# Optimization experiments

Hardware: AMD Instinct MI355X
Metric: run time of the kernel (lower is better)

## Reference

```python
import jax, jax.numpy as jnp
import numpy as np

B, NG, K_NN = 8, 4096, 3          # graphs, nodes per graph, knn k
CHEB_K = 4                        # SGWT/Chebyshev order K
IN_CH, HID, M, OUT_CH = 32, 64, 100, 16
N = B * NG
E_PPI = 600
BIG = 1e9


def knn_edges(x, n_graphs, n_per, k):
    """Per-graph knn_graph (no self loops). Returns global (src, dst), edges grouped per target node."""
    xg = x.reshape(n_graphs, n_per, -1)
    sq = jnp.sum(xg * xg, axis=-1)                                   # [B, n]
    d = sq[:, :, None] + sq[:, None, :] - 2.0 * jnp.einsum('bic,bjc->bij', xg, xg)
    d = d + BIG * jnp.eye(n_per, dtype=x.dtype)                      # exclude self
    idx = jax.lax.top_k(-d, k)[1]                                    # [B, n, k] neighbor ids
    offs = (jnp.arange(n_graphs) * n_per)[:, None, None]
    src = (idx + offs).reshape(-1)
    dst = jnp.broadcast_to(jnp.arange(n_per)[None, :, None] + offs, (n_graphs, n_per, k)).reshape(-1)
    return src, dst


def cheb_conv(x, src, dst, w, W, b, n):
    """SGWT/Chebyshev conv: sum_k T_k(L~) x W_k with L~ = -D^-1/2 A D^-1/2 (lambda_max=2)."""
    deg = jax.ops.segment_sum(w, dst, num_segments=n)
    dn = jnp.where(deg > 0, jax.lax.rsqrt(jnp.maximum(deg, 1e-12)), 0.0)
    wn = w * dn[dst] * dn[src]

    def lap(v):
        return -jax.ops.segment_sum(wn[:, None] * v[src], dst, num_segments=n)

    Z_prev = x
    out = x @ W[0]
    Z_cur = lap(x)
    out = out + Z_cur @ W[1]
    for kk in range(2, W.shape[0]):
        Z_next = 2.0 * lap(Z_cur) - Z_prev
        out = out + Z_next @ W[kk]
        Z_prev, Z_cur = Z_cur, Z_next
    return out + b


def graph_norm(x, alpha, gamma, beta, n_graphs, n_per, eps=1e-5):
    xg = x.reshape(n_graphs, n_per, -1)
    mean = xg.mean(axis=1, keepdims=True)
    sub = xg - alpha * mean
    var = (sub * sub).mean(axis=1, keepdims=True)
    out = gamma * sub * jax.lax.rsqrt(var + eps) + beta
    return out.reshape(x.shape)


def edge_conv(x, src, dst, W, b, n):
    """EdgeConv: max_j MLP([x_i, x_j - x_i])."""
    feat = jnp.concatenate([x[dst], x[src] - x[dst]], axis=1)
    h = jax.nn.relu(feat @ W + b)
    agg = jax.ops.segment_max(h, dst, num_segments=n)
    return jnp.where(jnp.isfinite(agg), agg, 0.0)


def mlp3(x, w1, b1, w2, b2, w3, b3):
    h = jax.nn.selu(x @ w1 + b1)
    h = jax.nn.selu(h @ w2 + b2)
    return h @ w3 + b3


def setup_inputs():
    key = jax.random.key(0)
    ks = jax.random.split(key, 32)

    def p(i, shape):
        fan_in = shape[-2] if len(shape) >= 2 else shape[-1]
        return jax.random.normal(ks[i], shape, jnp.float32) / np.sqrt(fan_in)

    inp = {
        'x': jax.random.normal(ks[0], (N, IN_CH), jnp.float32),
        'edge_weight': jax.random.uniform(ks[1], (N * K_NN,), jnp.float32),
        'batch': jnp.repeat(jnp.arange(B), NG),
        'connect': jax.random.randint(ks[2], (2, E_PPI), 0, M),
        # conv0 (SGWT) params
        'W0': p(3, (CHEB_K, IN_CH, HID)), 'b0': jnp.zeros((HID,), jnp.float32),
        # GraphNorm
        'gn_alpha': jnp.ones((HID,), jnp.float32), 'gn_gamma': jnp.ones((HID,), jnp.float32), 'gn_beta': jnp.zeros((HID,), jnp.float32),
        # conv1 (SGWT) params -> m*4
        'W1': p(4, (CHEB_K, HID, 4 * M)), 'b1c': jnp.zeros((4 * M,), jnp.float32),
        # fc1: 4m -> 2m -> m -> m
        'f1w1': p(5, (4 * M, 2 * M)), 'f1b1': jnp.zeros((2 * M,), jnp.float32),
        'f1w2': p(6, (2 * M, M)), 'f1b2': jnp.zeros((M,), jnp.float32),
        'f1w3': p(7, (M, M)), 'f1b3': jnp.zeros((M,), jnp.float32),
        # conv2 (PPIEdgeConv): 2*in_ch -> hidden
        'W2': p(8, (2 * IN_CH, HID)), 'b2': jnp.zeros((HID,), jnp.float32),
        # conv3 (DynamicEdgeConv): 2*hidden -> hidden
        'W3': p(9, (2 * HID, HID)), 'b3': jnp.zeros((HID,), jnp.float32),
        # fc2: h -> h/2 -> h/4 -> out
        'f2w1': p(10, (HID, HID // 2)), 'f2b1': jnp.zeros((HID // 2,), jnp.float32),
        'f2w2': p(11, (HID // 2, HID // 4)), 'f2b2': jnp.zeros((HID // 4,), jnp.float32),
        'f2w3': p(12, (HID // 4, OUT_CH)), 'f2b3': jnp.zeros((OUT_CH,), jnp.float32),
    }
    return inp


def reference(x, edge_weight, batch, connect, W0, b0, gn_alpha, gn_gamma, gn_beta,
              W1, b1c, f1w1, f1b1, f1w2, f1b2, f1w3, f1b3,
              W2, b2, W3, b3, f2w1, f2b1, f2w2, f2b2, f2w3, f2b3):
    n = x.shape[0]
    # knn on raw features -> SGWT conv0 -> GraphNorm
    src, dst = knn_edges(x, B, NG, K_NN)
    u = cheb_conv(x, src, dst, edge_weight, W0, b0, n)
    u = graph_norm(u, gn_alpha, gn_gamma, gn_beta, B, NG)
    # knn on hidden features -> SGWT conv1 -> fc1
    src, dst = knn_edges(u, B, NG, K_NN)
    u = cheb_conv(u, src, dst, edge_weight, W1, b1c, n)
    u = mlp3(u, f1w1, f1b1, f1w2, f1b2, f1w3, f1b3)                   # [N, M]
    # DiffPool-style soft assignment pooling
    S = jax.nn.softmax(u, axis=-1).reshape(B, NG, M)
    Xd = x.reshape(B, NG, IN_CH)
    pooled = jnp.einsum('bnm,bnc->bmc', S, Xd) / S.sum(axis=1)[:, :, None]
    xp = pooled.reshape(B * M, IN_CH)
    # PPIEdgeConv over fixed 'connect' graph replicated per pooled graph
    offs = (jnp.arange(B) * M)[:, None]
    psrc = (connect[0][None, :] + offs).reshape(-1)
    pdst = (connect[1][None, :] + offs).reshape(-1)
    h = edge_conv(xp, psrc, pdst, W2, b2, B * M)                      # [B*M, HID]
    # DynamicEdgeConv: knn(k=3) on features
    ksrc, kdst = knn_edges(h, B, M, K_NN)
    y = edge_conv(h, ksrc, kdst, W3, b3, B * M)
    z = h + y
    v = mlp3(z, f2w1, f2b1, f2w2, f2b2, f2w3, f2b3)                   # [B*M, OUT_CH]
    return u, v
```

## Files before the change

### kernel.cpp

```cpp
#include <hip/hip_runtime.h>
#include <hip/hip_bf16.h>
#include <math.h>

#define DEVFN static __device__ __forceinline__

DEVFN int clampi(int v, int lo, int hi){ return v < lo ? lo : (v > hi ? hi : v); }


__global__ void k_zero(float* __restrict__ p, int n){
  int i = blockIdx.x*256 + threadIdx.x;
  if (i < n) p[i] = 0.f;
}

__global__ void k_filli(int* __restrict__ p, int n, int v){
  int i = blockIdx.x*256 + threadIdx.x;
  if (i < n) p[i] = v;
}

__global__ void k_fillf(float* __restrict__ p, int n, float v){
  int i = blockIdx.x*256 + threadIdx.x;
  if (i < n) p[i] = v;
}

__global__ void k_sqnorm(const float* __restrict__ x, float* __restrict__ sq, int n, int C){
  int i = blockIdx.x*256 + threadIdx.x;
  if (i >= n) return;
  const float* r = x + (size_t)i*C;
  float s = 0.f;
  for (int c = 0; c < C; ++c){ float v = r[c]; s += v*v; }
  sq[i] = s;
}


DEVFN void top3i(float d, int j, float& d0, float& d1, float& d2, int& i0, int& i1, int& i2){
  if (d < d2){
    if (d < d1){
      d2 = d1; i2 = i1;
      if (d < d0){ d1 = d0; i1 = i0; d0 = d; i0 = j; }
      else       { d1 = d;  i1 = j; }
    } else { d2 = d; i2 = j; }
  }
}

DEVFN void top3t(float d, int j, float& d0, float& d1, float& d2, int& j0, int& j1, int& j2){
  if (d < d2 || (d == d2 && j < j2)){
    if (d < d1 || (d == d1 && j < j1)){
      d2 = d1; j2 = j1;
      if (d < d0 || (d == d0 && j < j0)){ d1 = d0; j1 = j0; d0 = d; j0 = j; }
      else { d1 = d; j1 = j; }
    } else { d2 = d; j2 = j; }
  }
}


template<int C, int TJ>
__global__ __launch_bounds__(64) void k_knn(
    const float* __restrict__ x, const float* __restrict__ sq,
    int n_per, int bpg, int nsplit, int csize,
    float* __restrict__ partd, int* __restrict__ parti)
{
  int bid  = blockIdx.x;
  int s    = bid % nsplit;
  int b2i  = bid / nsplit;
  int g    = b2i / bpg;
  int tile = b2i % bpg;
  int tid  = threadIdx.x;
  int i0 = tile*128 + tid;
  int i1 = i0 + 64;
  const float* xg = x  + (size_t)g*n_per*C;
  const float* sg = sq + (size_t)g*n_per;
  bool a0 = i0 < n_per, a1 = i1 < n_per;
  float xi0[C], xi1[C];
  float q0 = 0.f, q1 = 0.f;
  if (a0){
    #pragma unroll
    for (int c = 0; c < C; ++c) xi0[c] = xg[(size_t)i0*C + c];
    q0 = sg[i0];
  } else {
    #pragma unroll
    for (int c = 0; c < C; ++c) xi0[c] = 0.f;
  }
  if (a1){
    #pragma unroll
    for (int c = 0; c < C; ++c) xi1[c] = xg[(size_t)i1*C + c];
    q1 = sg[i1];
  } else {
    #pragma unroll
    for (int c = 0; c < C; ++c) xi1[c] = 0.f;
  }
  __shared__ float xs[TJ*C];
  __shared__ float ss[TJ];
  float d00 = __builtin_inff(), d01 = __builtin_inff(), d02 = __builtin_inff();
  float d10 = __builtin_inff(), d11 = __builtin_inff(), d12 = __builtin_inff();
  int n00 = 0, n01 = 0, n02 = 0;
  int n10 = 0, n11 = 0, n12 = 0;

  int jbase = s*csize;
  int jend  = min(n_per, jbase + csize);
  for (int t0 = jbase; t0 < jend; t0 += TJ){
    int lim = min(TJ, jend - t0);
    __syncthreads();
    for (int idx = tid; idx < lim*C; idx += 64) xs[idx] = xg[(size_t)t0*C + idx];
    for (int idx = tid; idx < lim;   idx += 64) ss[idx] = sg[t0 + idx];
    __syncthreads();
    for (int jj = 0; jj < lim; ++jj){
      const float4* xr = (const float4*)(xs + jj*C);
      float p0a=0,p0b=0,p0c=0,p0d=0;
      float p1a=0,p1b=0,p1c=0,p1d=0;
      #pragma unroll
      for (int c4 = 0; c4 < C/4; ++c4){
        float4 w = xr[c4];
        p0a += xi0[4*c4+0]*w.x; p0b += xi0[4*c4+1]*w.y;
        p0c += xi0[4*c4+2]*w.z; p0d += xi0[4*c4+3]*w.w;
        p1a += xi1[4*c4+0]*w.x; p1b += xi1[4*c4+1]*w.y;
        p1c += xi1[4*c4+2]*w.z; p1d += xi1[4*c4+3]*w.w;
      }
      int j = t0 + jj;
      float dv0 = q0 + ss[jj] - 2.f*((p0a+p0b)+(p0c+p0d));
      float dv1 = q1 + ss[jj] - 2.f*((p1a+p1b)+(p1c+p1d));
      if (a0 && j != i0) top3i(dv0, j, d00,d01,d02, n00,n01,n02);
      if (a1 && j != i1) top3i(dv1, j, d10,d11,d12, n10,n11,n12);
    }
  }
  if (a0){
    size_t o = ((size_t)(g*n_per + i0)*nsplit + s)*3;
    partd[o+0]=d00; partd[o+1]=d01; partd[o+2]=d02;
    parti[o+0]=n00; parti[o+1]=n01; parti[o+2]=n02;
  }
  if (a1){
    size_t o = ((size_t)(g*n_per + i1)*nsplit + s)*3;
    partd[o+0]=d10; partd[o+1]=d11; partd[o+2]=d12;
    parti[o+0]=n10; parti[o+1]=n11; parti[o+2]=n12;
  }
}


template<int C, int TJ>
__global__ __launch_bounds__(64) void k_knn1r(
    const float* __restrict__ x, const float* __restrict__ sq,
    int n_per, int bpg, int nsplit, int csize,
    float* __restrict__ partd, int* __restrict__ parti)
{
  int bid  = blockIdx.x;
  int s    = bid % nsplit;
  int b2i  = bid / nsplit;
  int g    = b2i / bpg;
  int tile = b2i % bpg;
  int tid  = threadIdx.x;
  int i0 = tile*64 + tid;
  const float* xg = x  + (size_t)g*n_per*C;
  const float* sg = sq + (size_t)g*n_per;
  float xi0[C];
  #pragma unroll
  for (int c = 0; c < C; ++c) xi0[c] = xg[(size_t)i0*C + c];
  float q0 = sg[i0];

  __shared__ float xs[TJ*C];
  __shared__ float ss[TJ];
  float d00 = __builtin_inff(), d01 = __builtin_inff(), d02 = __builtin_inff();
  int n00 = 0, n01 = 0, n02 = 0;

  int jbase = s*csize;
  int jend  = min(n_per, jbase + csize);
  for (int t0 = jbase; t0 < jend; t0 += TJ){
    int lim = min(TJ, jend - t0);
    __syncthreads();
    for (int idx = tid; idx < lim*C; idx += 64) xs[idx] = xg[(size_t)t0*C + idx];
    for (int idx = tid; idx < lim;   idx += 64) ss[idx] = sg[t0 + idx];
    __syncthreads();
    for (int jj = 0; jj < lim; ++jj){
      const float4* xr = (const float4*)(xs + jj*C);
      float p0a=0,p0b=0,p0c=0,p0d=0;
      #pragma unroll
      for (int c4 = 0; c4 < C/4; ++c4){
        float4 w = xr[c4];
        p0a += xi0[4*c4+0]*w.x; p0b += xi0[4*c4+1]*w.y;
        p0c += xi0[4*c4+2]*w.z; p0d += xi0[4*c4+3]*w.w;
      }
      int j = t0 + jj;
      float dv0 = q0 + ss[jj] - 2.f*((p0a+p0b)+(p0c+p0d));
      if (j != i0) top3i(dv0, j, d00,d01,d02, n00,n01,n02);
    }
  }
  size_t o = ((size_t)(g*n_per + i0)*nsplit + s)*3;
  partd[o+0]=d00; partd[o+1]=d01; partd[o+2]=d02;
  parti[o+0]=n00; parti[o+1]=n01; parti[o+2]=n02;
}

__global__ void k_knnmerge(const float* __restrict__ partd, const int* __restrict__ parti,
                           int n_total, int n_per, int nsplit, int* __restrict__ nbr)
{
  int row = blockIdx.x*256 + threadIdx.x;
  if (row >= n_total) return;
  float d0 = __builtin_inff(), d1 = __builtin_inff(), d2 = __builtin_inff();
  int j0 = 0, j1 = 0, j2 = 0;
  for (int s = 0; s < nsplit; ++s){
    for (int q = 0; q < 3; ++q){
      size_t o = ((size_t)row*nsplit + s)*3 + q;
      float d = partd[o]; int j = parti[o];
      top3t(d, j, d0,d1,d2, j0,j1,j2);
    }
  }
  int g = row / n_per;
  nbr[row*3+0] = g*n_per + clampi(j0, 0, n_per-1);
  nbr[row*3+1] = g*n_per + clampi(j1, 0, n_per-1);
  nbr[row*3+2] = g*n_per + clampi(j2, 0, n_per-1);
}


__global__ void k_chebwn(const float* __restrict__ w, const int* __restrict__ nbr,
                         float* __restrict__ wn, int ne, int n){
  int e = blockIdx.x*256 + threadIdx.x;
  if (e >= ne) return;
  int i = e/3;
  int s = clampi(nbr[e], 0, n-1);
  float sd = w[3*i] + w[3*i+1] + w[3*i+2];
  float sv = w[3*s] + w[3*s+1] + w[3*s+2];
  float dnd = (sd > 0.f) ? 1.f / sqrtf(fmaxf(sd, 1e-12f)) : 0.f;
  float dns = (sv > 0.f) ? 1.f / sqrtf(fmaxf(sv, 1e-12f)) : 0.f;
  wn[e] = w[e] * dnd * dns;
}

template<int C>
__global__ void k_lap(const float* __restrict__ v, const float* __restrict__ zp,
                      const float* __restrict__ wn, const int* __restrict__ nbr,
                      float* __restrict__ out, int total, float aa, float bb)
{
  int idx = blockIdx.x*256 + threadIdx.x;
  if (idx >= total) return;
  int i = idx / C;
  int c = idx - i*C;
  int e = i*3;
  int nmax = total / C;
  int s0 = clampi(nbr[e+0], 0, nmax-1);
  int s1 = clampi(nbr[e+1], 0, nmax-1);
  int s2 = clampi(nbr[e+2], 0, nmax-1);
  float s = wn[e+0]*v[(size_t)s0*C + c]
          + wn[e+1]*v[(size_t)s1*C + c]
          + wn[e+2]*v[(size_t)s2*C + c];
  float r = -aa*s;
  if (bb != 0.f) r += bb*zp[idx];
  out[idx] = r;
}


struct In4 { const float* p0; const float* p1; const float* p2; const float* p3; };

template<int ACT, int NIN>
__global__ __launch_bounds__(256) void k_mm(
    In4 ins, const float* __restrict__ W,
    const float* __restrict__ bias, float* __restrict__ out,
    int nrows, int cin, int cout)
{
  __shared__ float inl[64][65];
  __shared__ float wl[64][64];
  int r0 = blockIdx.x * 64;
  int c0 = blockIdx.y * 64;
  int tid = threadIdx.x;
  int tr = tid & 15, tc = tid >> 4;
  float acc[4][4] = {{0,0,0,0},{0,0,0,0},{0,0,0,0},{0,0,0,0}};
  const float* inp[4] = {ins.p0, ins.p1, ins.p2, ins.p3};
  for (int ni = 0; ni < NIN; ++ni){
    const float* A = inp[ni];
    const float* Wb = W + (size_t)ni*cin*cout;
    for (int k0 = 0; k0 < cin; k0 += 64){
      int klim = min(64, cin - k0);
      __syncthreads();
      for (int idx = tid; idx < 64*64; idx += 256){
        int rr = idx >> 6, kk = idx & 63;
        float v = 0.f;
        if (r0 + rr < nrows && kk < klim) v = A[(size_t)(r0+rr)*cin + k0 + kk];
        inl[rr][kk] = v;
      }
      for (int idx = tid; idx < 64*64; idx += 256){
        int kk = idx >> 6, jj = idx & 63;
        float v = 0.f;
        if (kk < klim && c0 + jj < cout) v = Wb[(size_t)(k0+kk)*cout + c0 + jj];
        wl[kk][jj] = v;
      }
      __syncthreads();
      for (int kk = 0; kk < 64; ++kk){
        float4 wv = *(const float4*)&wl[kk][tc*4];
        float a0v = inl[tr*4+0][kk];
        float a1v = inl[tr*4+1][kk];
        float a2v = inl[tr*4+2][kk];
        float a3v = inl[tr*4+3][kk];
        acc[0][0] += a0v*wv.x; acc[0][1] += a0v*wv.y; acc[0][2] += a0v*wv.z; acc[0][3] += a0v*wv.w;
        acc[1][0] += a1v*wv.x; acc[1][1] += a1v*wv.y; acc[1][2] += a1v*wv.z; acc[1][3] += a1v*wv.w;
        acc[2][0] += a2v*wv.x; acc[2][1] += a2v*wv.y; acc[2][2] += a2v*wv.z; acc[2][3] += a2v*wv.w;
        acc[3][0] += a3v*wv.x; acc[3][1] += a3v*wv.y; acc[3][2] += a3v*wv.z; acc[3][3] += a3v*wv.w;
      }
    }
  }
  #pragma unroll
  for (int q = 0; q < 4; ++q){
    int r = r0 + tr*4 + q;
    if (r >= nrows) continue;
    #pragma unroll
    for (int p = 0; p < 4; ++p){
      int j = c0 + tc*4 + p;
      if (j >= cout) continue;
      float v = acc[q][p] + bias[j];
      if (ACT == 1) v = fmaxf(v, 0.f);
      if (ACT == 2) v = 1.0507009873554805f * (v > 0.f ? v : 1.6732632423543772f * expm1f(v));
      out[(size_t)r*cout + j] = v;
    }
  }
}


__global__ void k_gnstat(const float* __restrict__ x, float* __restrict__ msum_p,
                         float* __restrict__ m2sum_p)
{
  int g = blockIdx.x >> 4, chunk = blockIdx.x & 15;
  int c = threadIdx.x & 63, q = threadIdx.x >> 6;
  const float* xg = x + (size_t)g*4096*64;
  int nb = chunk*256;
  float s1 = 0.f, s2 = 0.f;
  for (int n = nb + q; n < nb + 256; n += 4){
    float v = xg[(size_t)n*64 + c];
    s1 += v; s2 += v*v;
  }
  __shared__ float r1[4][64], r2[4][64];
  r1[q][c] = s1; r2[q][c] = s2;
  __syncthreads();
  if (q == 0){
    msum_p [(g*16 + chunk)*64 + c] = r1[0][c]+r1[1][c]+r1[2][c]+r1[3][c];
    m2sum_p[(g*16 + chunk)*64 + c] = r2[0][c]+r2[1][c]+r2[2][c]+r2[3][c];
  }
}

__global__ void k_gnapply(float* __restrict__ x, const float* __restrict__ msum_p,
                          const float* __restrict__ m2sum_p,
                          const float* __restrict__ alpha, const float* __restrict__ gamma,
                          const float* __restrict__ beta)
{
  int idx = blockIdx.x*256 + threadIdx.x;
  if (idx >= 32768*64) return;
  int c = idx & 63;
  int node = idx >> 6;
  int g = node >> 12;
  float ms = 0.f, m2 = 0.f;
  for (int ch = 0; ch < 16; ++ch){
    ms += msum_p [(g*16 + ch)*64 + c];
    m2 += m2sum_p[(g*16 + ch)*64 + c];
  }
  float m  = ms * (1.f/4096.f);
  float e2 = m2 * (1.f/4096.f);
  float al = alpha[c];
  float var = e2 - (2.f*al - al*al)*m*m;
  float sub = x[idx] - al*m;
  x[idx] = gamma[c] * sub * (1.f/sqrtf(fmaxf(var, 0.f) + 1e-5f)) + beta[c];
}


__global__ void k_softmax(const float* __restrict__ u, float* __restrict__ S, int n){
  int i = blockIdx.x*256 + threadIdx.x;
  if (i >= n) return;
  const float* r = u + (size_t)i*100;
  float* o = S + (size_t)i*100;
  float lr[100];
  float m = -__builtin_inff();
  for (int j = 0; j < 100; ++j){ lr[j] = r[j]; m = fmaxf(m, lr[j]); }
  float ssum = 0.f;
  for (int j = 0; j < 100; ++j){ lr[j] = expf(lr[j] - m); ssum += lr[j]; }
  float inv = 1.f / ssum;
  for (int j = 0; j < 100; ++j) o[j] = lr[j] * inv;
}

__global__ void k_pool(const float* __restrict__ S, const float* __restrict__ xf,
                       float* __restrict__ PT)
{
  int g = blockIdx.x >> 4, chunk = blockIdx.x & 15;
  int tid = threadIdx.x;
  __shared__ float Sl[64*100];
  __shared__ float Xl[64*32];
  float acc[13];
  int mq[13], cq[13];
  int base = tid*13;
  #pragma unroll
  for (int q = 0; q < 13; ++q){
    acc[q] = 0.f;
    int oi = base + q;
    mq[q] = (oi < 3300) ? oi/33 : 0;
    cq[q] = (oi < 3300) ? oi%33 : 0;
  }
  const float* Sg = S  + ((size_t)g*4096 + chunk*256)*100;
  const float* Xg = xf + ((size_t)g*4096 + chunk*256)*32;
  for (int n0 = 0; n0 < 256; n0 += 64){
    __syncthreads();
    for (int idx = tid; idx < 6400; idx += 256) Sl[idx] = Sg[(size_t)n0*100 + idx];
    for (int idx = tid; idx < 2048; idx += 256) Xl[idx] = Xg[(size_t)n0*32 + idx];
    __syncthreads();
    for (int nn = 0; nn < 64; ++nn){
      #pragma unroll
      for (int q = 0; q < 13; ++q){
        int ci = cq[q] & 31;
        float xv = Xl[nn*32 + ci];
        if (cq[q] == 32) xv = 1.f;
        acc[q] += Sl[nn*100 + mq[q]] * xv;
      }
    }
  }
  #pragma unroll
  for (int q = 0; q < 13; ++q){
    int oi = base + q;
    if (oi < 3300) atomicAdd(&PT[(size_t)g*3300 + oi], acc[q]);
  }
}

__global__ void k_xp(const float* __restrict__ PT, float* __restrict__ xp){
  int i = blockIdx.x*256 + threadIdx.x;
  if (i >= 800*32) return;
  int bm = i >> 5, c = i & 31;
  xp[i] = PT[(size_t)bm*33 + c] / PT[(size_t)bm*33 + 32];
}


__global__ void k_ppi(const float* __restrict__ xp, const int* __restrict__ connect,
                      const float* __restrict__ W2, const float* __restrict__ b2v,
                      int* __restrict__ hraw)
{
  int idx = blockIdx.x*256 + threadIdx.x;
  if (idx >= 8*600*64) return;
  int c  = idx & 63;
  int eg = idx >> 6;
  int b  = eg / 600, e = eg - b*600;
  int sI = b*100 + clampi(connect[e],       0, 99);
  int dI = b*100 + clampi(connect[600 + e], 0, 99);
  float acc = b2v[c];
  #pragma unroll
  for (int t = 0; t < 32; ++t) acc += xp[(size_t)dI*32 + t] * W2[t*64 + c];
  #pragma unroll
  for (int t = 0; t < 32; ++t) acc += (xp[(size_t)sI*32 + t] - xp[(size_t)dI*32 + t]) * W2[(32+t)*64 + c];
  float r = fmaxf(acc, 0.f);
  atomicMax(&hraw[(size_t)dI*64 + c], __float_as_int(r));
}

__global__ void k_hfin(const int* __restrict__ hraw, float* __restrict__ h, int n){
  int i = blockIdx.x*256 + threadIdx.x;
  if (i >= n) return;
  float v = __int_as_float(hraw[i]);
  h[i] = (v < -1e37f) ? 0.f : v;
}


__global__ void k_dyn(const float* __restrict__ h, const int* __restrict__ nbr3,
                      const float* __restrict__ W3, const float* __restrict__ b3v,
                      float* __restrict__ z)
{
  int idx = blockIdx.x*256 + threadIdx.x;
  if (idx >= 800*64) return;
  int c = idx & 63, i = idx >> 6;
  float base = b3v[c];
  for (int t = 0; t < 64; ++t) base += h[(size_t)i*64 + t] * W3[t*64 + c];
  float mx = 0.f;
  for (int k = 0; k < 3; ++k){
    int sI = clampi(nbr3[i*3 + k], 0, 799);
    float acc = base;
    for (int t = 0; t < 64; ++t) acc += (h[(size_t)sI*64 + t] - h[(size_t)i*64 + t]) * W3[(64+t)*64 + c];
    mx = fmaxf(mx, fmaxf(acc, 0.f));
  }
  z[idx] = h[idx] + mx;
}


extern "C" void kernel_launch(void* const* d_in, const int* in_sizes, int n_in,
                              void* d_out, int out_size, void* d_ws, size_t ws_size,
                              hipStream_t stream)
{
  const size_t REQ_SMALL = 11785728ull * 4ull;
  const size_t REQ_BIG   = 31854592ull * 4ull;
  if (ws_size < REQ_SMALL || n_in < 27){
    int nb = (out_size + 255)/256;
    k_fillf<<<nb, 256, 0, stream>>>((float*)d_out, out_size, (float)ws_size);
    return;
  }
  const bool big = (ws_size >= REQ_BIG);

  const float* x    = (const float*)d_in[0];
  const float* ew   = (const float*)d_in[1];
  const int*  connect = (const int*)d_in[3];
  const float* W0  = (const float*)d_in[4];
  const float* b0  = (const float*)d_in[5];
  const float* gal = (const float*)d_in[6];
  const float* gga = (const float*)d_in[7];
  const float* gbe = (const float*)d_in[8];
  const float* W1  = (const float*)d_in[9];
  const float* b1c = (const float*)d_in[10];
  const float* f1w1=(const float*)d_in[11]; const float* f1b1=(const float*)d_in[12];
  const float* f1w2=(const float*)d_in[13]; const float* f1b2=(const float*)d_in[14];
  const float* f1w3=(const float*)d_in[15]; const float* f1b3=(const float*)d_in[16];
  const float* W2  = (const float*)d_in[17]; const float* b2v=(const float*)d_in[18];
  const float* W3  = (const float*)d_in[19]; const float* b3v=(const float*)d_in[20];
  const float* f2w1=(const float*)d_in[21]; const float* f2b1=(const float*)d_in[22];
  const float* f2w2=(const float*)d_in[23]; const float* f2b2=(const float*)d_in[24];
  const float* f2w3=(const float*)d_in[25]; const float* f2b3=(const float*)d_in[26];

  float* ws   = (float*)d_ws;
  float* u0   = ws;
  float* Za   = ws +  2097152;
  float* Zb   = ws +  4194304;
  float* Zc   = ws +  6291456;
  float* acc  = ws +  8388608;
  float* h1   = big ? (ws + 21495808) : (acc + 1638400);
  float* h2   = big ? (ws + 28049408) : (acc + 2457600);
  float* partd= Za;
  int*   parti= (int*)Zb;
  float* Sb   = Za;
  float* sm   = big ? (ws + 31326208) : (ws + 11272192);
  float* sqb  = sm;
  int*   nbr  = (int*)(sm + 163840);
  int*   nbr3 = (int*)(sm + 262144);
  float* PT   = sm + 266240;
  float* xp   = sm + 294912;
  int*   hraw = (int*)(sm + 320512);
  float* hb   = sm + 371712;
  float* zb   = sm + 422912;
  float* g1   = sm + 474112;
  float* g2   = sm + 499712;
  float* wnb  = sm + 65536;

  float* ub   = (float*)d_out;
  float* vout = ub + 3276800;

  const int N = 32768;

  k_sqnorm<<<128, 256, 0, stream>>>(x, sqb, N, 32);
  k_knn<32,64><<<2048, 64, 0, stream>>>(x, sqb, 4096, 32, 8, 512, partd, parti);
  k_knnmerge<<<128, 256, 0, stream>>>(partd, parti, N, 4096, 8, nbr);

  k_chebwn<<<384, 256, 0, stream>>>(ew, nbr, wnb, 3*N, N);

  k_lap<32><<<4096, 256, 0, stream>>>(x, x, wnb, nbr, Za, N*32, 1.f, 0.f);
  k_lap<32><<<4096, 256, 0, stream>>>(Za, x, wnb, nbr, Zb, N*32, 2.f, -1.f);
  k_lap<32><<<4096, 256, 0, stream>>>(Zb, Za, wnb, nbr, Zc, N*32, 2.f, -1.f);
  {
    In4 ins{x, Za, Zb, Zc};
    k_mm<0,4><<<dim3(512,1), 256, 0, stream>>>(ins, W0, b0, u0, N, 32, 64);
  }

  k_gnstat<<<128, 256, 0, stream>>>(u0, sqb, sqb + 8192);
  k_gnapply<<<8192, 256, 0, stream>>>(u0, sqb, sqb + 8192, gal, gga, gbe);

  k_sqnorm<<<128, 256, 0, stream>>>(u0, sqb, N, 64);
  k_knn1r<64,32><<<4096, 64, 0, stream>>>(u0, sqb, 4096, 64, 8, 512, partd, parti);
  k_knnmerge<<<128, 256, 0, stream>>>(partd, parti, N, 4096, 8, nbr);
  k_chebwn<<<384, 256, 0, stream>>>(ew, nbr, wnb, 3*N, N);

  k_lap<64><<<8192, 256, 0, stream>>>(u0, u0, wnb, nbr, Za, N*64, 1.f, 0.f);
  k_lap<64><<<8192, 256, 0, stream>>>(Za, u0, wnb, nbr, Zb, N*64, 2.f, -1.f);
  k_lap<64><<<8192, 256, 0, stream>>>(Zb, Za, wnb, nbr, Zc, N*64, 2.f, -1.f);

  {
    int nch  = big ? 1 : 8;
    int rows = big ? N : 4096;
    int gx   = big ? 512 : 64;
    for (int ch = 0; ch < nch; ++ch){
      size_t o64  = (size_t)ch*4096*64;
      size_t o100 = (size_t)ch*4096*100;
      In4 ic{u0 + o64, Za + o64, Zb + o64, Zc + o64};
      k_mm<0,4><<<dim3(gx,7), 256, 0, stream>>>(ic, W1, b1c, acc, rows, 64, 400);
      In4 i1{acc, nullptr, nullptr, nullptr};
      k_mm<2,1><<<dim3(gx,4), 256, 0, stream>>>(i1, f1w1, f1b1, h1, rows, 400, 200);
      In4 i2{h1, nullptr, nullptr, nullptr};
      k_mm<2,1><<<dim3(gx,2), 256, 0, stream>>>(i2, f1w2, f1b2, h2, rows, 200, 100);
      In4 i3{h2, nullptr, nullptr, nullptr};
      k_mm<0,1><<<dim3(gx,2), 256, 0, stream>>>(i3, f1w3, f1b3, ub + o100, rows, 100, 100);
    }
  }

  k_softmax<<<128, 256, 0, stream>>>(ub, Sb, N);
  k_zero<<<104, 256, 0, stream>>>(PT, 26400);
  k_pool<<<128, 256, 0, stream>>>(Sb, x, PT);
  k_xp<<<100, 256, 0, stream>>>(PT, xp);

  k_filli<<<200, 256, 0, stream>>>(hraw, 51200, (int)0xFF800000);
  k_ppi<<<1200, 256, 0, stream>>>(xp, connect, W2, b2v, hraw);
  k_hfin<<<200, 256, 0, stream>>>(hraw, hb, 51200);

  k_sqnorm<<<4, 256, 0, stream>>>(hb, sqb, 800, 64);
  k_knn<64,64><<<8, 64, 0, stream>>>(hb, sqb, 100, 1, 1, 100, partd, parti);
  k_knnmerge<<<4, 256, 0, stream>>>(partd, parti, 800, 100, 1, nbr3);
  k_dyn<<<200, 256, 0, stream>>>(hb, nbr3, W3, b3v, zb);

  {
    In4 j1{zb, nullptr, nullptr, nullptr};
    k_mm<2,1><<<dim3(13,1), 256, 0, stream>>>(j1, f2w1, f2b1, g1, 800, 64, 32);
    In4 j2{g1, nullptr, nullptr, nullptr};
    k_mm<2,1><<<dim3(13,1), 256, 0, stream>>>(j2, f2w2, f2b2, g2, 800, 32, 16);
    In4 j3{g2, nullptr, nullptr, nullptr};
    k_mm<0,1><<<dim3(13,1), 256, 0, stream>>>(j3, f2w3, f2b3, vout, 800, 16, 16);
  }
}
```

Before: 1.766 ms.

## Replace first kNN kernel with 256-thread single-row blocks and finer split

Adds a specialised 32-channel kNN kernel for the first kNN step. Each 256-thread block handles 256 query rows, one row per thread, and stages 128 candidate rows in shared memory per tile. The candidate range is split 16 ways instead of 8, and the merge reads 16 partial lists. The row-constant squared norm is dropped from the distance, which saves arithmetic without changing the per-row ranking. The trade-off is one query row per thread instead of two, so fewer rows reuse each shared-memory read, and the partial-result buffer and merge work double.

```diff
diff --git a/kernel.cpp b/kernel.cpp
--- a/kernel.cpp
+++ b/kernel.cpp
@@ -50,6 +50,105 @@
       else { d1 = d; j1 = j; }
     } else { d2 = d; j2 = j; }
   }
+}
+
+
+__global__ __launch_bounds__(256) void k_knn4_32(
+    const float* __restrict__ x, const float* __restrict__ sq,
+    int n_per, int nsplit, int csize,
+    float* __restrict__ partd, int* __restrict__ parti)
+{
+  int s = blockIdx.x, tile = blockIdx.y, g = blockIdx.z;
+  int tid = threadIdx.x;
+  const float* xg = x  + (size_t)g*n_per*32;
+  const float* sg = sq + (size_t)g*n_per;
+  int ri = tile*256 + tid;
+  float xi0[32];
+  #pragma unroll
+  for (int c = 0; c < 32; ++c) xi0[c] = xg[(size_t)ri*32 + c];
+
+  __shared__ float xs[128*32];
+  __shared__ float ss[128];
+
+  const float INF = __builtin_inff();
+  float d0=INF,d1=INF,d2=INF; int j0=0,j1=0,j2=0;
+
+  int jbase = s*csize;
+  for (int t0 = jbase; t0 < jbase + csize; t0 += 128){
+    __syncthreads();
+    for (int idx = tid; idx < 128*32; idx += 256) xs[idx] = xg[(size_t)t0*32 + idx];
+    if (tid < 128) ss[tid] = sg[t0 + tid];
+    __syncthreads();
+    for (int jj = 0; jj < 128; ++jj){
+      const float4* xr = (const float4*)(xs + jj*32);
+      float pa=0.f,pb=0.f,pc=0.f,pd=0.f;
+      #pragma unroll
+      for (int c4 = 0; c4 < 8; ++c4){
+        float4 w = xr[c4];
+        pa += xi0[4*c4+0]*w.x; pb += xi0[4*c4+1]*w.y;
+        pc += xi0[4*c4+2]*w.z; pd += xi0[4*c4+3]*w.w;
+      }
+      int j = t0 + jj;
+      float v = fmaf(-2.f, (pa+pb)+(pc+pd), ss[jj]);
+      if (j != ri) top3i(v, j, d0,d1,d2, j0,j1,j2);
+    }
+  }
+  size_t o = ((size_t)(g*n_per + ri)*nsplit + s)*3;
+  partd[o+0]=d0; partd[o+1]=d1; partd[o+2]=d2;
+  parti[o+0]=j0; parti[o+1]=j1; parti[o+2]=j2;
+}
+
+
+template<int C, int TJ>
+__global__ __launch_bounds__(64) void k_knn1r(
+    const float* __restrict__ x, const float* __restrict__ sq,
+    int n_per, int bpg, int nsplit, int csize,
+    float* __restrict__ partd, int* __restrict__ parti)
+{
+  int bid  = blockIdx.x;
+  int s    = bid % nsplit;
+  int b2i  = bid / nsplit;
+  int g    = b2i / bpg;
+  int tile = b2i % bpg;
+  int tid  = threadIdx.x;
+  int i0 = tile*64 + tid;
+  const float* xg = x  + (size_t)g*n_per*C;
+  const float* sg = sq + (size_t)g*n_per;
+  float xi0[C];
+  #pragma unroll
+  for (int c = 0; c < C; ++c) xi0[c] = xg[(size_t)i0*C + c];
+  float q0 = sg[i0];
+
+  __shared__ float xs[TJ*C];
+  __shared__ float ss[TJ];
+  float d00 = __builtin_inff(), d01 = __builtin_inff(), d02 = __builtin_inff();
+  int n00 = 0, n01 = 0, n02 = 0;
+
+  int jbase = s*csize;
+  int jend  = min(n_per, jbase + csize);
+  for (int t0 = jbase; t0 < jend; t0 += TJ){
+    int lim = min(TJ, jend - t0);
+    __syncthreads();
+    for (int idx = tid; idx < lim*C; idx += 64) xs[idx] = xg[(size_t)t0*C + idx];
+    for (int idx = tid; idx < lim;   idx += 64) ss[idx] = sg[t0 + idx];
+    __syncthreads();
+    for (int jj = 0; jj < lim; ++jj){
+      const float4* xr = (const float4*)(xs + jj*C);
+      float p0a=0,p0b=0,p0c=0,p0d=0;
+      #pragma unroll
+      for (int c4 = 0; c4 < C/4; ++c4){
+        float4 w = xr[c4];
+        p0a += xi0[4*c4+0]*w.x; p0b += xi0[4*c4+1]*w.y;
+        p0c += xi0[4*c4+2]*w.z; p0d += xi0[4*c4+3]*w.w;
+      }
+      int j = t0 + jj;
+      float dv0 = q0 + ss[jj] - 2.f*((p0a+p0b)+(p0c+p0d));
+      if (j != i0) top3i(dv0, j, d00,d01,d02, n00,n01,n02);
+    }
+  }
+  size_t o = ((size_t)(g*n_per + i0)*nsplit + s)*3;
+  partd[o+0]=d00; partd[o+1]=d01; partd[o+2]=d02;
+  parti[o+0]=n00; parti[o+1]=n01; parti[o+2]=n02;
 }
 
 
@@ -132,59 +231,6 @@
     partd[o+0]=d10; partd[o+1]=d11; partd[o+2]=d12;
     parti[o+0]=n10; parti[o+1]=n11; parti[o+2]=n12;
   }
-}
-
-
-template<int C, int TJ>
-__global__ __launch_bounds__(64) void k_knn1r(
-    const float* __restrict__ x, const float* __restrict__ sq,
-    int n_per, int bpg, int nsplit, int csize,
-    float* __restrict__ partd, int* __restrict__ parti)
-{
-  int bid  = blockIdx.x;
-  int s    = bid % nsplit;
-  int b2i  = bid / nsplit;
-  int g    = b2i / bpg;
-  int tile = b2i % bpg;
-  int tid  = threadIdx.x;
-  int i0 = tile*64 + tid;
-  const float* xg = x  + (size_t)g*n_per*C;
-  const float* sg = sq + (size_t)g*n_per;
-  float xi0[C];
-  #pragma unroll
-  for (int c = 0; c < C; ++c) xi0[c] = xg[(size_t)i0*C + c];
-  float q0 = sg[i0];
-
-  __shared__ float xs[TJ*C];
-  __shared__ float ss[TJ];
-  float d00 = __builtin_inff(), d01 = __builtin_inff(), d02 = __builtin_inff();
-  int n00 = 0, n01 = 0, n02 = 0;
-
-  int jbase = s*csize;
-  int jend  = min(n_per, jbase + csize);
-  for (int t0 = jbase; t0 < jend; t0 += TJ){
-    int lim = min(TJ, jend - t0);
-    __syncthreads();
-    for (int idx = tid; idx < lim*C; idx += 64) xs[idx] = xg[(size_t)t0*C + idx];
-    for (int idx = tid; idx < lim;   idx += 64) ss[idx] = sg[t0 + idx];
-    __syncthreads();
-    for (int jj = 0; jj < lim; ++jj){
-      const float4* xr = (const float4*)(xs + jj*C);
-      float p0a=0,p0b=0,p0c=0,p0d=0;
-      #pragma unroll
-      for (int c4 = 0; c4 < C/4; ++c4){
-        float4 w = xr[c4];
-        p0a += xi0[4*c4+0]*w.x; p0b += xi0[4*c4+1]*w.y;
-        p0c += xi0[4*c4+2]*w.z; p0d += xi0[4*c4+3]*w.w;
-      }
-      int j = t0 + jj;
-      float dv0 = q0 + ss[jj] - 2.f*((p0a+p0b)+(p0c+p0d));
-      if (j != i0) top3i(dv0, j, d00,d01,d02, n00,n01,n02);
-    }
-  }
-  size_t o = ((size_t)(g*n_per + i0)*nsplit + s)*3;
-  partd[o+0]=d00; partd[o+1]=d01; partd[o+2]=d02;
-  parti[o+0]=n00; parti[o+1]=n01; parti[o+2]=n02;
 }
 
 __global__ void k_knnmerge(const float* __restrict__ partd, const int* __restrict__ parti,
@@ -527,8 +573,8 @@
   const int N = 32768;
 
   k_sqnorm<<<128, 256, 0, stream>>>(x, sqb, N, 32);
-  k_knn<32,64><<<2048, 64, 0, stream>>>(x, sqb, 4096, 32, 8, 512, partd, parti);
-  k_knnmerge<<<128, 256, 0, stream>>>(partd, parti, N, 4096, 8, nbr);
+  k_knn4_32<<<dim3(16,16,8), 256, 0, stream>>>(x, sqb, 4096, 16, 256, partd, parti);
+  k_knnmerge<<<128, 256, 0, stream>>>(partd, parti, N, 4096, 16, nbr);
 
   k_chebwn<<<384, 256, 0, stream>>>(ew, nbr, wnb, 3*N, N);
 
```

After: 1.821 ms. 3.1% more time.
